# Kernel optimization log

Measured on AMD Instinct MI355X. Metric: run time of the kernel, lower is better.

Reference implementation:

```python
import jax, jax.numpy as jnp
import numpy as np

N_NODES = 100000
N_EDGES = 1600000
IN_DIM = 128
HID = 64
CONV2_OUT = 8
GLOBAL_DIM = 24
OUT_DIM = 1
NUM_GRAPHS = 64
NEG_SLOPE = 0.01


def setup_inputs() -> dict:
    key = jax.random.key(0)
    ks = jax.random.split(key, 12)
    x = jax.random.normal(ks[0], (N_NODES, IN_DIM), dtype=jnp.float32)
    edge_index = jax.random.randint(ks[1], (2, N_EDGES), 0, N_NODES, dtype=jnp.int32)
    batch = jnp.sort(jax.random.randint(ks[2], (N_NODES,), 0, NUM_GRAPHS, dtype=jnp.int32))
    global_features = jax.random.normal(ks[3], (NUM_GRAPHS, GLOBAL_DIM), dtype=jnp.float32)
    # GCNConv weights (glorot-ish scale) and Linear weights
    W1 = jax.random.normal(ks[4], (IN_DIM, HID), dtype=jnp.float32) / np.sqrt(IN_DIM)
    b1 = jnp.zeros((HID,), dtype=jnp.float32)
    W2 = jax.random.normal(ks[5], (HID, CONV2_OUT), dtype=jnp.float32) / np.sqrt(HID)
    b2 = jnp.zeros((CONV2_OUT,), dtype=jnp.float32)
    fcW1 = jax.random.normal(ks[6], (GLOBAL_DIM + CONV2_OUT, 16), dtype=jnp.float32) / np.sqrt(GLOBAL_DIM + CONV2_OUT)
    fcb1 = jnp.zeros((16,), dtype=jnp.float32)
    fcW2 = jax.random.normal(ks[7], (16, OUT_DIM), dtype=jnp.float32) / np.sqrt(16)
    fcb2 = jnp.zeros((OUT_DIM,), dtype=jnp.float32)
    return {"x": x, "edge_index": edge_index, "batch": batch,
            "global_features": global_features,
            "W1": W1, "b1": b1, "W2": W2, "b2": b2,
            "fcW1": fcW1, "fcb1": fcb1, "fcW2": fcW2, "fcb2": fcb2}


def gcn_conv(x, src, dst, W, b):
    """PyG GCNConv: add self-loops, sym-normalize, aggregate x@W from src->dst."""
    n = x.shape[0]
    h = x @ W  # [N, F_out]
    loop = jnp.arange(n, dtype=src.dtype)
    src2 = jnp.concatenate([src, loop])
    dst2 = jnp.concatenate([dst, loop])
    deg = jax.ops.segment_sum(jnp.ones_like(dst2, dtype=h.dtype), dst2, num_segments=n)
    dinv = jnp.where(deg > 0, jax.lax.rsqrt(deg), 0.0)
    norm = dinv[src2] * dinv[dst2]  # [E+N]
    msg = h[src2] * norm[:, None]   # edge gather (dominant traffic)
    out = jax.ops.segment_sum(msg, dst2, num_segments=n)
    return out + b


def reference(x, edge_index, batch, global_features, W1, b1, W2, b2, fcW1, fcb1, fcW2, fcb2):
    src, dst = edge_index[0], edge_index[1]
    h = jax.nn.leaky_relu(gcn_conv(x, src, dst, W1, b1), NEG_SLOPE)
    h = jax.nn.leaky_relu(gcn_conv(h, src, dst, W2, b2), NEG_SLOPE)
    # global mean pool over graphs
    sums = jax.ops.segment_sum(h, batch, num_segments=NUM_GRAPHS)
    cnts = jax.ops.segment_sum(jnp.ones((h.shape[0],), h.dtype), batch, num_segments=NUM_GRAPHS)
    pool = sums / jnp.maximum(cnts, 1.0)[:, None]
    z = jnp.concatenate([pool, global_features], axis=1)
    z = jax.nn.leaky_relu(z @ fcW1 + fcb1, NEG_SLOPE)
    z = jax.nn.leaky_relu(z @ fcW2 + fcb2, NEG_SLOPE)
    return z
```

## Files before the change

kernel.cpp:

```cpp
#include <hip/hip_runtime.h>

constexpr int N_NODES = 100000;
constexpr int N_EDGES = 1600000;
constexpr int IN_DIM  = 128;
constexpr int HID     = 64;
constexpr int C2      = 8;
constexpr int GDIM    = 24;
constexpr int NG      = 64;
constexpr float SLOPE = 0.01f;
constexpr int NB_SCAN = (N_NODES + 255) / 256;

__device__ __forceinline__ float lrelu(float v) { return v > 0.f ? v : SLOPE * v; }

__device__ __forceinline__ float bflo(unsigned int u) { return __uint_as_float(u << 16); }
__device__ __forceinline__ float bfhi(unsigned int u) { return __uint_as_float(u & 0xffff0000u); }
__device__ __forceinline__ unsigned short f2bf(float f) {
    unsigned int i = __float_as_uint(f);
    unsigned int r = (i + 0x7fffu + ((i >> 16) & 1u)) >> 16;
    return (unsigned short)r;
}

__global__ void k_rank(const int* __restrict__ dst, int* __restrict__ deg,
                       int* __restrict__ rnk) {
    int t = blockIdx.x * 256 + threadIdx.x;
    if (t < N_EDGES / 4) {
        int4 d = ((const int4*)dst)[t];
        int4 r;
        r.x = atomicAdd(&deg[d.x], 1);
        r.y = atomicAdd(&deg[d.y], 1);
        r.z = atomicAdd(&deg[d.z], 1);
        r.w = atomicAdd(&deg[d.w], 1);
        ((int4*)rnk)[t] = r;
    }
}

__global__ void k_scan1(const int* __restrict__ deg, int* __restrict__ rowptr,
                        int* __restrict__ bsum, float* __restrict__ dinv) {
    __shared__ int s[256];
    int tid = threadIdx.x;
    int i = blockIdx.x * 256 + tid;
    int v = (i < N_NODES) ? deg[i] : 0;
    if (i < N_NODES) dinv[i] = rsqrtf((float)(v + 1));
    s[tid] = v;
    __syncthreads();
    for (int off = 1; off < 256; off <<= 1) {
        int t = (tid >= off) ? s[tid - off] : 0;
        __syncthreads();
        s[tid] += t;
        __syncthreads();
    }
    if (i < N_NODES) rowptr[i] = s[tid] - v;
    if (tid == 255) bsum[blockIdx.x] = s[255];
}

__global__ void k_scan2(const int* __restrict__ bsum, int* __restrict__ bsumx) {
    __shared__ int s[512];
    int tid = threadIdx.x;
    int v = (tid < NB_SCAN) ? bsum[tid] : 0;
    s[tid] = v;
    __syncthreads();
    for (int off = 1; off < 512; off <<= 1) {
        int t = (tid >= off) ? s[tid - off] : 0;
        __syncthreads();
        s[tid] += t;
        __syncthreads();
    }
    if (tid < NB_SCAN) bsumx[tid] = s[tid] - v;
}

__global__ void k_place(const int* __restrict__ src, const int* __restrict__ dst,
                        const int* __restrict__ rnk, const int* __restrict__ rowptr,
                        const int* __restrict__ bsumx, int* __restrict__ eidx) {
    int t = blockIdx.x * 256 + threadIdx.x;
    if (t < N_EDGES / 4) {
        int4 d = ((const int4*)dst)[t];
        int4 r = ((const int4*)rnk)[t];
        int4 s = ((const int4*)src)[t];
        int px = rowptr[d.x] + bsumx[d.x >> 8] + r.x;
        int py = rowptr[d.y] + bsumx[d.y >> 8] + r.y;
        int pz = rowptr[d.z] + bsumx[d.z >> 8] + r.z;
        int pw = rowptr[d.w] + bsumx[d.w >> 8] + r.w;
        eidx[px] = s.x; eidx[py] = s.y; eidx[pz] = s.z; eidx[pw] = s.w;
    }
}

__global__ __launch_bounds__(256) void k_gemm1(const float* __restrict__ x,
                                               const float* __restrict__ W1,
                                               const float* __restrict__ dinv,
                                               unsigned short* __restrict__ hs1) {
    __shared__ float sW[IN_DIM * HID];
    __shared__ float sX[32][IN_DIM];
    int node0 = blockIdx.x * 32;
    for (int t = threadIdx.x; t < IN_DIM * HID / 4; t += 256)
        ((float4*)sW)[t] = ((const float4*)W1)[t];
    for (int t = threadIdx.x; t < 32 * IN_DIM / 4; t += 256) {
        int r = t >> 5, c4 = t & 31;
        ((float4*)&sX[r][0])[c4] = ((const float4*)(x + (size_t)(node0 + r) * IN_DIM))[c4];
    }
    __syncthreads();
    int col = threadIdx.x & 63;
    int nb  = (threadIdx.x >> 6) * 8;
    float acc[8] = {0.f, 0.f, 0.f, 0.f, 0.f, 0.f, 0.f, 0.f};
    for (int k4 = 0; k4 < IN_DIM; k4 += 4) {
        float w0 = sW[(k4 + 0) * HID + col];
        float w1 = sW[(k4 + 1) * HID + col];
        float w2 = sW[(k4 + 2) * HID + col];
        float w3 = sW[(k4 + 3) * HID + col];
#pragma unroll
        for (int j = 0; j < 8; ++j) {
            float4 xv = *((const float4*)&sX[nb + j][k4]);
            acc[j] += xv.x * w0 + xv.y * w1 + xv.z * w2 + xv.w * w3;
        }
    }
#pragma unroll
    for (int j = 0; j < 8; ++j) {
        int n = node0 + nb + j;
        hs1[(size_t)n * HID + col] = f2bf(acc[j] * dinv[n]);
    }
}

__global__ __launch_bounds__(256) void k_agg1(const int* __restrict__ rowptr,
                                              const int* __restrict__ bsumx,
                                              const int* __restrict__ deg,
                                              const int* __restrict__ eidx,
                                              const unsigned short* __restrict__ hs1,
                                              const float* __restrict__ dinv,
                                              const float* __restrict__ b1,
                                              const float* __restrict__ W2,
                                              float* __restrict__ hs2) {
    int node = blockIdx.x * 4 + (threadIdx.x >> 6);
    int lane = threadIdx.x & 63;
    int q    = lane & 7;
    int slot = lane >> 3;
    float w2f[8];
#pragma unroll
    for (int i = 0; i < 8; ++i) w2f[i] = W2[(8 * q + i) * C2 + slot];
    int start = rowptr[node] + bsumx[node >> 8];
    int cnt   = deg[node];
    uint4 hv = ((const uint4*)(hs1 + (size_t)node * HID))[q];
    float acc[8] = {0.f, 0.f, 0.f, 0.f, 0.f, 0.f, 0.f, 0.f};
    for (int base = 0; base < cnt; base += 64) {
        int idx = (base + lane < cnt) ? eidx[start + base + lane] : 0;
        int lim = min(64, cnt - base);
        int trips = (lim + 15) >> 4;
        for (int t = 0; t < trips; ++t) {
            int k0 = slot + t * 16;
            int k1 = k0 + 8;
            int s0 = __shfl(idx, k0);
            int s1 = __shfl(idx, k1 & 63);
            uint4 v0 = ((const uint4*)(hs1 + (size_t)s0 * HID))[q];
            uint4 v1 = ((const uint4*)(hs1 + (size_t)s1 * HID))[q];
            if (k0 >= lim) { v0.x = 0; v0.y = 0; v0.z = 0; v0.w = 0; }
            if (k1 >= lim) { v1.x = 0; v1.y = 0; v1.z = 0; v1.w = 0; }
            acc[0] += bflo(v0.x); acc[1] += bfhi(v0.x);
            acc[2] += bflo(v0.y); acc[3] += bfhi(v0.y);
            acc[4] += bflo(v0.z); acc[5] += bfhi(v0.z);
            acc[6] += bflo(v0.w); acc[7] += bfhi(v0.w);
            acc[0] += bflo(v1.x); acc[1] += bfhi(v1.x);
            acc[2] += bflo(v1.y); acc[3] += bfhi(v1.y);
            acc[4] += bflo(v1.z); acc[5] += bfhi(v1.z);
            acc[6] += bflo(v1.w); acc[7] += bfhi(v1.w);
        }
    }
#pragma unroll
    for (int m = 8; m < 64; m <<= 1)
#pragma unroll
        for (int i = 0; i < 8; ++i) acc[i] += __shfl_xor(acc[i], m);
    float self[8] = {bflo(hv.x), bfhi(hv.x), bflo(hv.y), bfhi(hv.y),
                     bflo(hv.z), bfhi(hv.z), bflo(hv.w), bfhi(hv.w)};
    float di = dinv[node];
    float4 bb0 = ((const float4*)b1)[2 * q];
    float4 bb1 = ((const float4*)b1)[2 * q + 1];
    float bv[8] = {bb0.x, bb0.y, bb0.z, bb0.w, bb1.x, bb1.y, bb1.z, bb1.w};
    float p = 0.f;
#pragma unroll
    for (int i = 0; i < 8; ++i) {
        float y = lrelu(di * (acc[i] + self[i]) + bv[i]);
        p += y * w2f[i];
    }
#pragma unroll
    for (int m = 1; m < 8; m <<= 1) p += __shfl_xor(p, m);
    if (q == 0) hs2[(size_t)node * C2 + slot] = p * di;
}

__global__ __launch_bounds__(256) void k_agg2(const int* __restrict__ rowptr,
                                              const int* __restrict__ bsumx,
                                              const int* __restrict__ deg,
                                              const int* __restrict__ eidx,
                                              const float* __restrict__ hs2,
                                              const float* __restrict__ dinv,
                                              const float* __restrict__ b2,
                                              float* __restrict__ y2) {
    int node = blockIdx.x * 4 + (threadIdx.x >> 6);
    int lane = threadIdx.x & 63;
    int q    = lane & 1;
    int slot = lane >> 1;
    int start = rowptr[node] + bsumx[node >> 8];
    int cnt   = deg[node];
    float4 acc = make_float4(0.f, 0.f, 0.f, 0.f);
    for (int base = 0; base < cnt; base += 64) {
        int idx = (base + lane < cnt) ? eidx[start + base + lane] : 0;
        int lim = min(64, cnt - base);
        int s0 = __shfl(idx, slot);
        int s1 = __shfl(idx, slot + 32);
        float4 v0 = ((const float4*)(hs2 + (size_t)s0 * C2))[q];
        float4 v1 = ((const float4*)(hs2 + (size_t)s1 * C2))[q];
        if (slot >= lim)      { v0.x = 0.f; v0.y = 0.f; v0.z = 0.f; v0.w = 0.f; }
        if (slot + 32 >= lim) { v1.x = 0.f; v1.y = 0.f; v1.z = 0.f; v1.w = 0.f; }
        acc.x += v0.x + v1.x; acc.y += v0.y + v1.y;
        acc.z += v0.z + v1.z; acc.w += v0.w + v1.w;
    }
    for (int m = 2; m < 64; m <<= 1) {
        acc.x += __shfl_xor(acc.x, m); acc.y += __shfl_xor(acc.y, m);
        acc.z += __shfl_xor(acc.z, m); acc.w += __shfl_xor(acc.w, m);
    }
    if (slot == 0) {
        float4 h = ((const float4*)(hs2 + (size_t)node * C2))[q];
        float di = dinv[node];
        const float* bb = b2 + q * 4;
        float4 r;
        r.x = lrelu(di * (acc.x + h.x) + bb[0]);
        r.y = lrelu(di * (acc.y + h.y) + bb[1]);
        r.z = lrelu(di * (acc.z + h.z) + bb[2]);
        r.w = lrelu(di * (acc.w + h.w) + bb[3]);
        ((float4*)(y2 + (size_t)node * C2))[q] = r;
    }
}

__device__ __forceinline__ int lower_bound(const int* __restrict__ b, int n, int v) {
    int lo = 0, hi = n;
    while (lo < hi) {
        int m = (lo + hi) >> 1;
        if (b[m] < v) lo = m + 1; else hi = m;
    }
    return lo;
}

__global__ __launch_bounds__(256) void k_pool(const float* __restrict__ y2,
                                              const int* __restrict__ batch,
                                              const float* __restrict__ gfeat,
                                              const float* __restrict__ fcW1,
                                              const float* __restrict__ fcb1,
                                              const float* __restrict__ fcW2,
                                              const float* __restrict__ fcb2,
                                              float* __restrict__ out) {
    __shared__ float s[256];
    int g   = blockIdx.x;
    int tid = threadIdx.x;
    int start = lower_bound(batch, N_NODES, g);
    int end   = lower_bound(batch, N_NODES, g + 1);
    int col = tid & 7;
    float local = 0.f;
    for (int n = start + (tid >> 3); n < end; n += 32)
        local += y2[(size_t)n * C2 + col];
    s[tid] = local;
    __syncthreads();
    for (int off = 128; off >= 8; off >>= 1) {
        if (tid < off) s[tid] += s[tid + off];
        __syncthreads();
    }
    if (tid == 0) {
        float cnt = fmaxf((float)(end - start), 1.f);
        float z[C2 + GDIM];
        for (int c = 0; c < C2; ++c) z[c] = s[c] / cnt;
        for (int c = 0; c < GDIM; ++c) z[C2 + c] = gfeat[g * GDIM + c];
        float acc2 = fcb2[0];
        for (int j = 0; j < 16; ++j) {
            float acc = fcb1[j];
            for (int c = 0; c < C2 + GDIM; ++c) acc += z[c] * fcW1[c * 16 + j];
            acc2 += lrelu(acc) * fcW2[j];
        }
        out[g] = lrelu(acc2);
    }
}

extern "C" void kernel_launch(void* const* d_in, const int* in_sizes, int n_in,
                              void* d_out, int out_size, void* d_ws, size_t ws_size,
                              hipStream_t stream) {
    const float* x     = (const float*)d_in[0];
    const int*   ei    = (const int*)d_in[1];
    const int*   batch = (const int*)d_in[2];
    const float* gfeat = (const float*)d_in[3];
    const float* W1    = (const float*)d_in[4];
    const float* b1    = (const float*)d_in[5];
    const float* W2    = (const float*)d_in[6];
    const float* b2    = (const float*)d_in[7];
    const float* fcW1  = (const float*)d_in[8];
    const float* fcb1  = (const float*)d_in[9];
    const float* fcW2  = (const float*)d_in[10];
    const float* fcb2  = (const float*)d_in[11];
    const int* src = ei;
    const int* dst = ei + N_EDGES;

    char* ws = (char*)d_ws;
    size_t off = 0;
    auto alloc = [&](size_t bytes) -> void* {
        void* p = ws + off;
        off = (off + bytes + 255) & ~(size_t)255;
        return p;
    };
    int*   deg    = (int*)  alloc((size_t)N_NODES * 4);
    float* dinv   = (float*)alloc((size_t)N_NODES * 4);
    int*   rowptr = (int*)  alloc((size_t)N_NODES * 4);
    int*   bsum   = (int*)  alloc(512 * 4);
    int*   bsumx  = (int*)  alloc(512 * 4);
    int*   rnk    = (int*)  alloc((size_t)N_EDGES * 4);
    int*   eidx   = (int*)  alloc((size_t)N_EDGES * 4);
    unsigned short* hs1 = (unsigned short*)alloc((size_t)N_NODES * HID * 2);
    float* hs2    = (float*)alloc((size_t)N_NODES * C2 * 4);
    float* y2     = (float*)alloc((size_t)N_NODES * C2 * 4);

    hipMemsetAsync(deg, 0, (size_t)N_NODES * 4, stream);

    k_rank <<<(N_EDGES / 4 + 255) / 256, 256, 0, stream>>>(dst, deg, rnk);
    k_scan1<<<NB_SCAN, 256, 0, stream>>>(deg, rowptr, bsum, dinv);
    k_scan2<<<1, 512, 0, stream>>>(bsum, bsumx);
    k_place<<<(N_EDGES / 4 + 255) / 256, 256, 0, stream>>>(src, dst, rnk, rowptr, bsumx, eidx);

    k_gemm1<<<N_NODES / 32, 256, 0, stream>>>(x, W1, dinv, hs1);
    k_agg1 <<<N_NODES / 4, 256, 0, stream>>>(rowptr, bsumx, deg, eidx, hs1, dinv, b1, W2, hs2);
    k_agg2 <<<N_NODES / 4, 256, 0, stream>>>(rowptr, bsumx, deg, eidx, hs2, dinv, b2, y2);
    k_pool <<<NG, 256, 0, stream>>>(y2, batch, gfeat, fcW1, fcb1, fcW2, fcb2, (float*)d_out);
}
```

Measured before the change: 283.9 us.

## Merge degree ranking with GEMM1 and edge placement with bf16 scaling

The edge rank/degree atomics now share a launch with the X@W1 GEMM, which no longer depends on dinv and writes unscaled fp32 output to a scratch buffer. A second combined kernel performs CSR edge placement alongside a vectorized pass that scales rows by dinv and packs them to bf16. The aim is to overlap atomic-bound and compute-bound work and to cut the number of kernel launches. The cost is an extra fp32 round trip of N×64 floats (about 25.6 MB written and read again). The GEMM also stops staging X in shared memory, and hs2/y2 now alias the scratch buffer.

Result: slower. 338.4 us (+19.2%).

```diff
diff --git a/kernel.cpp b/kernel.cpp
--- a/kernel.cpp
+++ b/kernel.cpp
@@ -9,29 +9,62 @@
 constexpr int NG      = 64;
 constexpr float SLOPE = 0.01f;
 constexpr int NB_SCAN = (N_NODES + 255) / 256;
+constexpr int RANK_BLOCKS  = (N_EDGES / 4 + 255) / 256;
+constexpr int GEMM_BLOCKS  = N_NODES / 32;
+constexpr int PLACE_BLOCKS = RANK_BLOCKS;
+constexpr int SCALE_BLOCKS = N_NODES * HID / 8 / 256;
 
 __device__ __forceinline__ float lrelu(float v) { return v > 0.f ? v : SLOPE * v; }
 
 __device__ __forceinline__ float bflo(unsigned int u) { return __uint_as_float(u << 16); }
 __device__ __forceinline__ float bfhi(unsigned int u) { return __uint_as_float(u & 0xffff0000u); }
-__device__ __forceinline__ unsigned short f2bf(float f) {
+__device__ __forceinline__ unsigned int f2bf_u(float f) {
     unsigned int i = __float_as_uint(f);
-    unsigned int r = (i + 0x7fffu + ((i >> 16) & 1u)) >> 16;
-    return (unsigned short)r;
-}
-
-__global__ void k_rank(const int* __restrict__ dst, int* __restrict__ deg,
-                       int* __restrict__ rnk) {
-    int t = blockIdx.x * 256 + threadIdx.x;
-    if (t < N_EDGES / 4) {
-        int4 d = ((const int4*)dst)[t];
-        int4 r;
-        r.x = atomicAdd(&deg[d.x], 1);
-        r.y = atomicAdd(&deg[d.y], 1);
-        r.z = atomicAdd(&deg[d.z], 1);
-        r.w = atomicAdd(&deg[d.w], 1);
-        ((int4*)rnk)[t] = r;
-    }
+    return (i + 0x7fffu + ((i >> 16) & 1u)) >> 16;
+}
+
+__global__ __launch_bounds__(256) void k_front(const float* __restrict__ x,
+                                               const float* __restrict__ W1,
+                                               const int* __restrict__ dst,
+                                               int* __restrict__ deg,
+                                               int* __restrict__ rnk,
+                                               float* __restrict__ raw) {
+    __shared__ float sW[IN_DIM * HID];
+    if (blockIdx.x < RANK_BLOCKS) {
+        int t = blockIdx.x * 256 + threadIdx.x;
+        if (t < N_EDGES / 4) {
+            int4 d = ((const int4*)dst)[t];
+            int4 r;
+            r.x = atomicAdd(&deg[d.x], 1);
+            r.y = atomicAdd(&deg[d.y], 1);
+            r.z = atomicAdd(&deg[d.z], 1);
+            r.w = atomicAdd(&deg[d.w], 1);
+            ((int4*)rnk)[t] = r;
+        }
+        return;
+    }
+    int node0 = (blockIdx.x - RANK_BLOCKS) * 32;
+    for (int t = threadIdx.x; t < IN_DIM * HID / 4; t += 256)
+        ((float4*)sW)[t] = ((const float4*)W1)[t];
+    __syncthreads();
+    int col = threadIdx.x & 63;
+    int nb  = (threadIdx.x >> 6) * 8;
+    const float* xb = x + (size_t)(node0 + nb) * IN_DIM;
+    float acc[8] = {0.f, 0.f, 0.f, 0.f, 0.f, 0.f, 0.f, 0.f};
+    for (int k4 = 0; k4 < IN_DIM; k4 += 4) {
+        float w0 = sW[(k4 + 0) * HID + col];
+        float w1 = sW[(k4 + 1) * HID + col];
+        float w2 = sW[(k4 + 2) * HID + col];
+        float w3 = sW[(k4 + 3) * HID + col];
+#pragma unroll
+        for (int j = 0; j < 8; ++j) {
+            float4 xv = *((const float4*)(xb + (size_t)j * IN_DIM + k4));
+            acc[j] += xv.x * w0 + xv.y * w1 + xv.z * w2 + xv.w * w3;
+        }
+    }
+#pragma unroll
+    for (int j = 0; j < 8; ++j)
+        raw[(size_t)(node0 + nb + j) * HID + col] = acc[j];
 }
 
 __global__ void k_scan1(const int* __restrict__ deg, int* __restrict__ rowptr,
@@ -68,55 +101,40 @@
     if (tid < NB_SCAN) bsumx[tid] = s[tid] - v;
 }
 
-__global__ void k_place(const int* __restrict__ src, const int* __restrict__ dst,
-                        const int* __restrict__ rnk, const int* __restrict__ rowptr,
-                        const int* __restrict__ bsumx, int* __restrict__ eidx) {
-    int t = blockIdx.x * 256 + threadIdx.x;
-    if (t < N_EDGES / 4) {
-        int4 d = ((const int4*)dst)[t];
-        int4 r = ((const int4*)rnk)[t];
-        int4 s = ((const int4*)src)[t];
-        int px = rowptr[d.x] + bsumx[d.x >> 8] + r.x;
-        int py = rowptr[d.y] + bsumx[d.y >> 8] + r.y;
-        int pz = rowptr[d.z] + bsumx[d.z >> 8] + r.z;
-        int pw = rowptr[d.w] + bsumx[d.w >> 8] + r.w;
-        eidx[px] = s.x; eidx[py] = s.y; eidx[pz] = s.z; eidx[pw] = s.w;
-    }
-}
-
-__global__ __launch_bounds__(256) void k_gemm1(const float* __restrict__ x,
-                                               const float* __restrict__ W1,
-                                               const float* __restrict__ dinv,
-                                               unsigned short* __restrict__ hs1) {
-    __shared__ float sW[IN_DIM * HID];
-    __shared__ float sX[32][IN_DIM];
-    int node0 = blockIdx.x * 32;
-    for (int t = threadIdx.x; t < IN_DIM * HID / 4; t += 256)
-        ((float4*)sW)[t] = ((const float4*)W1)[t];
-    for (int t = threadIdx.x; t < 32 * IN_DIM / 4; t += 256) {
-        int r = t >> 5, c4 = t & 31;
-        ((float4*)&sX[r][0])[c4] = ((const float4*)(x + (size_t)(node0 + r) * IN_DIM))[c4];
-    }
-    __syncthreads();
-    int col = threadIdx.x & 63;
-    int nb  = (threadIdx.x >> 6) * 8;
-    float acc[8] = {0.f, 0.f, 0.f, 0.f, 0.f, 0.f, 0.f, 0.f};
-    for (int k4 = 0; k4 < IN_DIM; k4 += 4) {
-        float w0 = sW[(k4 + 0) * HID + col];
-        float w1 = sW[(k4 + 1) * HID + col];
-        float w2 = sW[(k4 + 2) * HID + col];
-        float w3 = sW[(k4 + 3) * HID + col];
-#pragma unroll
-        for (int j = 0; j < 8; ++j) {
-            float4 xv = *((const float4*)&sX[nb + j][k4]);
-            acc[j] += xv.x * w0 + xv.y * w1 + xv.z * w2 + xv.w * w3;
-        }
-    }
-#pragma unroll
-    for (int j = 0; j < 8; ++j) {
-        int n = node0 + nb + j;
-        hs1[(size_t)n * HID + col] = f2bf(acc[j] * dinv[n]);
-    }
+__global__ __launch_bounds__(256) void k_mid(const int* __restrict__ src,
+                                             const int* __restrict__ dst,
+                                             const int* __restrict__ rnk,
+                                             const int* __restrict__ rowptr,
+                                             const int* __restrict__ bsumx,
+                                             int* __restrict__ eidx,
+                                             const float* __restrict__ raw,
+                                             const float* __restrict__ dinv,
+                                             unsigned short* __restrict__ hs1) {
+    if (blockIdx.x < PLACE_BLOCKS) {
+        int t = blockIdx.x * 256 + threadIdx.x;
+        if (t < N_EDGES / 4) {
+            int4 d = ((const int4*)dst)[t];
+            int4 r = ((const int4*)rnk)[t];
+            int4 s = ((const int4*)src)[t];
+            int px = rowptr[d.x] + bsumx[d.x >> 8] + r.x;
+            int py = rowptr[d.y] + bsumx[d.y >> 8] + r.y;
+            int pz = rowptr[d.z] + bsumx[d.z >> 8] + r.z;
+            int pw = rowptr[d.w] + bsumx[d.w >> 8] + r.w;
+            eidx[px] = s.x; eidx[py] = s.y; eidx[pz] = s.z; eidx[pw] = s.w;
+        }
+        return;
+    }
+    int t = (blockIdx.x - PLACE_BLOCKS) * 256 + threadIdx.x;
+    int node = t >> 3;
+    float di = dinv[node];
+    float4 a = ((const float4*)raw)[2 * t];
+    float4 b = ((const float4*)raw)[2 * t + 1];
+    uint4 o;
+    o.x = f2bf_u(a.x * di) | (f2bf_u(a.y * di) << 16);
+    o.y = f2bf_u(a.z * di) | (f2bf_u(a.w * di) << 16);
+    o.z = f2bf_u(b.x * di) | (f2bf_u(b.y * di) << 16);
+    o.w = f2bf_u(b.z * di) | (f2bf_u(b.w * di) << 16);
+    ((uint4*)hs1)[t] = o;
 }
 
 __global__ __launch_bounds__(256) void k_agg1(const int* __restrict__ rowptr,
@@ -307,17 +325,17 @@
     int*   rnk    = (int*)  alloc((size_t)N_EDGES * 4);
     int*   eidx   = (int*)  alloc((size_t)N_EDGES * 4);
     unsigned short* hs1 = (unsigned short*)alloc((size_t)N_NODES * HID * 2);
-    float* hs2    = (float*)alloc((size_t)N_NODES * C2 * 4);
-    float* y2     = (float*)alloc((size_t)N_NODES * C2 * 4);
+    float* raw    = (float*)alloc((size_t)N_NODES * HID * 4);
+    float* hs2 = raw;
+    float* y2  = raw + (size_t)N_NODES * C2;
 
     hipMemsetAsync(deg, 0, (size_t)N_NODES * 4, stream);
 
-    k_rank <<<(N_EDGES / 4 + 255) / 256, 256, 0, stream>>>(dst, deg, rnk);
+    k_front<<<RANK_BLOCKS + GEMM_BLOCKS, 256, 0, stream>>>(x, W1, dst, deg, rnk, raw);
     k_scan1<<<NB_SCAN, 256, 0, stream>>>(deg, rowptr, bsum, dinv);
     k_scan2<<<1, 512, 0, stream>>>(bsum, bsumx);
-    k_place<<<(N_EDGES / 4 + 255) / 256, 256, 0, stream>>>(src, dst, rnk, rowptr, bsumx, eidx);
-
-    k_gemm1<<<N_NODES / 32, 256, 0, stream>>>(x, W1, dinv, hs1);
+    k_mid  <<<PLACE_BLOCKS + SCALE_BLOCKS, 256, 0, stream>>>(src, dst, rnk, rowptr, bsumx,
+                                                             eidx, raw, dinv, hs1);
     k_agg1 <<<N_NODES / 4, 256, 0, stream>>>(rowptr, bsumx, deg, eidx, hs1, dinv, b1, W2, hs2);
     k_agg2 <<<N_NODES / 4, 256, 0, stream>>>(rowptr, bsumx, deg, eidx, hs2, dinv, b2, y2);
     k_pool <<<NG, 256, 0, stream>>>(y2, batch, gfeat, fcW1, fcb1, fcW2, fcb2, (float*)d_out);
```

## Fuse CSR scan via atomic block offsets and process eight nodes per wavefront

Applied to the files above, without the earlier changes.

The two-pass prefix scan becomes a single pass. Each block claims its base offset with an atomicAdd on a global counter, so the second scan kernel and the per-block sum lookups in the place and aggregation kernels go away. Row segments are still disjoint but are no longer in node order, which can reduce locality of the edge index reads. Separately, each wavefront in both aggregation kernels now handles eight nodes in a loop rather than one, cutting the block count eightfold. That trades launch and scheduling overhead against less parallelism and more load imbalance per wavefront.

Result: faster. 262.9 us (-7.4%).

```diff
diff --git a/kernel.cpp b/kernel.cpp
--- a/kernel.cpp
+++ b/kernel.cpp
@@ -20,26 +20,27 @@
     return (unsigned short)r;
 }
 
-__global__ void k_rank(const int* __restrict__ dst, int* __restrict__ deg,
+__global__ void k_rank(const int* __restrict__ dst, int* __restrict__ cnt,
                        int* __restrict__ rnk) {
     int t = blockIdx.x * 256 + threadIdx.x;
     if (t < N_EDGES / 4) {
         int4 d = ((const int4*)dst)[t];
         int4 r;
-        r.x = atomicAdd(&deg[d.x], 1);
-        r.y = atomicAdd(&deg[d.y], 1);
-        r.z = atomicAdd(&deg[d.z], 1);
-        r.w = atomicAdd(&deg[d.w], 1);
+        r.x = atomicAdd(&cnt[d.x], 1);
+        r.y = atomicAdd(&cnt[d.y], 1);
+        r.z = atomicAdd(&cnt[d.z], 1);
+        r.w = atomicAdd(&cnt[d.w], 1);
         ((int4*)rnk)[t] = r;
     }
 }
 
-__global__ void k_scan1(const int* __restrict__ deg, int* __restrict__ rowptr,
-                        int* __restrict__ bsum, float* __restrict__ dinv) {
+__global__ void k_scan1(const int* __restrict__ cnt, int* __restrict__ rowptr,
+                        float* __restrict__ dinv, int* __restrict__ gbase) {
     __shared__ int s[256];
+    __shared__ int base;
     int tid = threadIdx.x;
     int i = blockIdx.x * 256 + tid;
-    int v = (i < N_NODES) ? deg[i] : 0;
+    int v = (i < N_NODES) ? cnt[i] : 0;
     if (i < N_NODES) dinv[i] = rsqrtf((float)(v + 1));
     s[tid] = v;
     __syncthreads();
@@ -49,38 +50,23 @@
         s[tid] += t;
         __syncthreads();
     }
-    if (i < N_NODES) rowptr[i] = s[tid] - v;
-    if (tid == 255) bsum[blockIdx.x] = s[255];
-}
-
-__global__ void k_scan2(const int* __restrict__ bsum, int* __restrict__ bsumx) {
-    __shared__ int s[512];
-    int tid = threadIdx.x;
-    int v = (tid < NB_SCAN) ? bsum[tid] : 0;
-    s[tid] = v;
+    if (tid == 255) base = atomicAdd(gbase, s[255]);
     __syncthreads();
-    for (int off = 1; off < 512; off <<= 1) {
-        int t = (tid >= off) ? s[tid - off] : 0;
-        __syncthreads();
-        s[tid] += t;
-        __syncthreads();
-    }
-    if (tid < NB_SCAN) bsumx[tid] = s[tid] - v;
+    if (i < N_NODES) rowptr[i] = base + s[tid] - v;
 }
 
 __global__ void k_place(const int* __restrict__ src, const int* __restrict__ dst,
                         const int* __restrict__ rnk, const int* __restrict__ rowptr,
-                        const int* __restrict__ bsumx, int* __restrict__ eidx) {
+                        int* __restrict__ eidx) {
     int t = blockIdx.x * 256 + threadIdx.x;
     if (t < N_EDGES / 4) {
         int4 d = ((const int4*)dst)[t];
         int4 r = ((const int4*)rnk)[t];
         int4 s = ((const int4*)src)[t];
-        int px = rowptr[d.x] + bsumx[d.x >> 8] + r.x;
-        int py = rowptr[d.y] + bsumx[d.y >> 8] + r.y;
-        int pz = rowptr[d.z] + bsumx[d.z >> 8] + r.z;
-        int pw = rowptr[d.w] + bsumx[d.w >> 8] + r.w;
-        eidx[px] = s.x; eidx[py] = s.y; eidx[pz] = s.z; eidx[pw] = s.w;
+        eidx[rowptr[d.x] + r.x] = s.x;
+        eidx[rowptr[d.y] + r.y] = s.y;
+        eidx[rowptr[d.z] + r.z] = s.z;
+        eidx[rowptr[d.w] + r.w] = s.w;
     }
 }
 
@@ -120,7 +106,6 @@
 }
 
 __global__ __launch_bounds__(256) void k_agg1(const int* __restrict__ rowptr,
-                                              const int* __restrict__ bsumx,
                                               const int* __restrict__ deg,
                                               const int* __restrict__ eidx,
                                               const unsigned short* __restrict__ hs1,
@@ -128,102 +113,109 @@
                                               const float* __restrict__ b1,
                                               const float* __restrict__ W2,
                                               float* __restrict__ hs2) {
-    int node = blockIdx.x * 4 + (threadIdx.x >> 6);
     int lane = threadIdx.x & 63;
     int q    = lane & 7;
     int slot = lane >> 3;
     float w2f[8];
 #pragma unroll
     for (int i = 0; i < 8; ++i) w2f[i] = W2[(8 * q + i) * C2 + slot];
-    int start = rowptr[node] + bsumx[node >> 8];
-    int cnt   = deg[node];
-    uint4 hv = ((const uint4*)(hs1 + (size_t)node * HID))[q];
-    float acc[8] = {0.f, 0.f, 0.f, 0.f, 0.f, 0.f, 0.f, 0.f};
-    for (int base = 0; base < cnt; base += 64) {
-        int idx = (base + lane < cnt) ? eidx[start + base + lane] : 0;
-        int lim = min(64, cnt - base);
-        int trips = (lim + 15) >> 4;
-        for (int t = 0; t < trips; ++t) {
-            int k0 = slot + t * 16;
-            int k1 = k0 + 8;
-            int s0 = __shfl(idx, k0);
-            int s1 = __shfl(idx, k1 & 63);
-            uint4 v0 = ((const uint4*)(hs1 + (size_t)s0 * HID))[q];
-            uint4 v1 = ((const uint4*)(hs1 + (size_t)s1 * HID))[q];
-            if (k0 >= lim) { v0.x = 0; v0.y = 0; v0.z = 0; v0.w = 0; }
-            if (k1 >= lim) { v1.x = 0; v1.y = 0; v1.z = 0; v1.w = 0; }
-            acc[0] += bflo(v0.x); acc[1] += bfhi(v0.x);
-            acc[2] += bflo(v0.y); acc[3] += bfhi(v0.y);
-            acc[4] += bflo(v0.z); acc[5] += bfhi(v0.z);
-            acc[6] += bflo(v0.w); acc[7] += bfhi(v0.w);
-            acc[0] += bflo(v1.x); acc[1] += bfhi(v1.x);
-            acc[2] += bflo(v1.y); acc[3] += bfhi(v1.y);
-            acc[4] += bflo(v1.z); acc[5] += bfhi(v1.z);
-            acc[6] += bflo(v1.w); acc[7] += bfhi(v1.w);
-        }
-    }
-#pragma unroll
-    for (int m = 8; m < 64; m <<= 1)
-#pragma unroll
-        for (int i = 0; i < 8; ++i) acc[i] += __shfl_xor(acc[i], m);
-    float self[8] = {bflo(hv.x), bfhi(hv.x), bflo(hv.y), bfhi(hv.y),
-                     bflo(hv.z), bfhi(hv.z), bflo(hv.w), bfhi(hv.w)};
-    float di = dinv[node];
     float4 bb0 = ((const float4*)b1)[2 * q];
     float4 bb1 = ((const float4*)b1)[2 * q + 1];
     float bv[8] = {bb0.x, bb0.y, bb0.z, bb0.w, bb1.x, bb1.y, bb1.z, bb1.w};
-    float p = 0.f;
-#pragma unroll
-    for (int i = 0; i < 8; ++i) {
-        float y = lrelu(di * (acc[i] + self[i]) + bv[i]);
-        p += y * w2f[i];
-    }
-#pragma unroll
-    for (int m = 1; m < 8; m <<= 1) p += __shfl_xor(p, m);
-    if (q == 0) hs2[(size_t)node * C2 + slot] = p * di;
+    int node_base = blockIdx.x * 32 + (threadIdx.x >> 6) * 8;
+
+    for (int nn = 0; nn < 8; ++nn) {
+        int node  = node_base + nn;
+        int start = rowptr[node];
+        int cnt   = deg[node];
+        uint4 hv = ((const uint4*)(hs1 + (size_t)node * HID))[q];
+        float acc[8] = {0.f, 0.f, 0.f, 0.f, 0.f, 0.f, 0.f, 0.f};
+        for (int base = 0; base < cnt; base += 64) {
+            int idx = (base + lane < cnt) ? eidx[start + base + lane] : 0;
+            int lim = min(64, cnt - base);
+            int trips = (lim + 15) >> 4;
+            for (int t = 0; t < trips; ++t) {
+                int k0 = slot + t * 16;
+                int k1 = k0 + 8;
+                int s0 = __shfl(idx, k0);
+                int s1 = __shfl(idx, k1 & 63);
+                uint4 v0 = ((const uint4*)(hs1 + (size_t)s0 * HID))[q];
+                uint4 v1 = ((const uint4*)(hs1 + (size_t)s1 * HID))[q];
+                if (k0 >= lim) { v0.x = 0; v0.y = 0; v0.z = 0; v0.w = 0; }
+                if (k1 >= lim) { v1.x = 0; v1.y = 0; v1.z = 0; v1.w = 0; }
+                acc[0] += bflo(v0.x); acc[1] += bfhi(v0.x);
+                acc[2] += bflo(v0.y); acc[3] += bfhi(v0.y);
+                acc[4] += bflo(v0.z); acc[5] += bfhi(v0.z);
+                acc[6] += bflo(v0.w); acc[7] += bfhi(v0.w);
+                acc[0] += bflo(v1.x); acc[1] += bfhi(v1.x);
+                acc[2] += bflo(v1.y); acc[3] += bfhi(v1.y);
+                acc[4] += bflo(v1.z); acc[5] += bfhi(v1.z);
+                acc[6] += bflo(v1.w); acc[7] += bfhi(v1.w);
+            }
+        }
+#pragma unroll
+        for (int m = 8; m < 64; m <<= 1)
+#pragma unroll
+            for (int i = 0; i < 8; ++i) acc[i] += __shfl_xor(acc[i], m);
+        float self[8] = {bflo(hv.x), bfhi(hv.x), bflo(hv.y), bfhi(hv.y),
+                         bflo(hv.z), bfhi(hv.z), bflo(hv.w), bfhi(hv.w)};
+        float di = dinv[node];
+        float p = 0.f;
+#pragma unroll
+        for (int i = 0; i < 8; ++i) {
+            float y = lrelu(di * (acc[i] + self[i]) + bv[i]);
+            p += y * w2f[i];
+        }
+#pragma unroll
+        for (int m = 1; m < 8; m <<= 1) p += __shfl_xor(p, m);
+        if (q == 0) hs2[(size_t)node * C2 + slot] = p * di;
+    }
 }
 
 __global__ __launch_bounds__(256) void k_agg2(const int* __restrict__ rowptr,
-                                              const int* __restrict__ bsumx,
                                               const int* __restrict__ deg,
                                               const int* __restrict__ eidx,
                                               const float* __restrict__ hs2,
                                               const float* __restrict__ dinv,
                                               const float* __restrict__ b2,
                                               float* __restrict__ y2) {
-    int node = blockIdx.x * 4 + (threadIdx.x >> 6);
     int lane = threadIdx.x & 63;
     int q    = lane & 1;
     int slot = lane >> 1;
-    int start = rowptr[node] + bsumx[node >> 8];
-    int cnt   = deg[node];
-    float4 acc = make_float4(0.f, 0.f, 0.f, 0.f);
-    for (int base = 0; base < cnt; base += 64) {
-        int idx = (base + lane < cnt) ? eidx[start + base + lane] : 0;
-        int lim = min(64, cnt - base);
-        int s0 = __shfl(idx, slot);
-        int s1 = __shfl(idx, slot + 32);
-        float4 v0 = ((const float4*)(hs2 + (size_t)s0 * C2))[q];
-        float4 v1 = ((const float4*)(hs2 + (size_t)s1 * C2))[q];
-        if (slot >= lim)      { v0.x = 0.f; v0.y = 0.f; v0.z = 0.f; v0.w = 0.f; }
-        if (slot + 32 >= lim) { v1.x = 0.f; v1.y = 0.f; v1.z = 0.f; v1.w = 0.f; }
-        acc.x += v0.x + v1.x; acc.y += v0.y + v1.y;
-        acc.z += v0.z + v1.z; acc.w += v0.w + v1.w;
-    }
-    for (int m = 2; m < 64; m <<= 1) {
-        acc.x += __shfl_xor(acc.x, m); acc.y += __shfl_xor(acc.y, m);
-        acc.z += __shfl_xor(acc.z, m); acc.w += __shfl_xor(acc.w, m);
-    }
-    if (slot == 0) {
-        float4 h = ((const float4*)(hs2 + (size_t)node * C2))[q];
-        float di = dinv[node];
-        const float* bb = b2 + q * 4;
-        float4 r;
-        r.x = lrelu(di * (acc.x + h.x) + bb[0]);
-        r.y = lrelu(di * (acc.y + h.y) + bb[1]);
-        r.z = lrelu(di * (acc.z + h.z) + bb[2]);
-        r.w = lrelu(di * (acc.w + h.w) + bb[3]);
-        ((float4*)(y2 + (size_t)node * C2))[q] = r;
+    int node_base = blockIdx.x * 32 + (threadIdx.x >> 6) * 8;
+
+    for (int nn = 0; nn < 8; ++nn) {
+        int node  = node_base + nn;
+        int start = rowptr[node];
+        int cnt   = deg[node];
+        float4 acc = make_float4(0.f, 0.f, 0.f, 0.f);
+        for (int base = 0; base < cnt; base += 64) {
+            int idx = (base + lane < cnt) ? eidx[start + base + lane] : 0;
+            int lim = min(64, cnt - base);
+            int s0 = __shfl(idx, slot);
+            int s1 = __shfl(idx, slot + 32);
+            float4 v0 = ((const float4*)(hs2 + (size_t)s0 * C2))[q];
+            float4 v1 = ((const float4*)(hs2 + (size_t)s1 * C2))[q];
+            if (slot >= lim)      { v0.x = 0.f; v0.y = 0.f; v0.z = 0.f; v0.w = 0.f; }
+            if (slot + 32 >= lim) { v1.x = 0.f; v1.y = 0.f; v1.z = 0.f; v1.w = 0.f; }
+            acc.x += v0.x + v1.x; acc.y += v0.y + v1.y;
+            acc.z += v0.z + v1.z; acc.w += v0.w + v1.w;
+        }
+        for (int m = 2; m < 64; m <<= 1) {
+            acc.x += __shfl_xor(acc.x, m); acc.y += __shfl_xor(acc.y, m);
+            acc.z += __shfl_xor(acc.z, m); acc.w += __shfl_xor(acc.w, m);
+        }
+        if (slot == 0) {
+            float4 h = ((const float4*)(hs2 + (size_t)node * C2))[q];
+            float di = dinv[node];
+            const float* bb = b2 + q * 4;
+            float4 r;
+            r.x = lrelu(di * (acc.x + h.x) + bb[0]);
+            r.y = lrelu(di * (acc.y + h.y) + bb[1]);
+            r.z = lrelu(di * (acc.z + h.z) + bb[2]);
+            r.w = lrelu(di * (acc.w + h.w) + bb[3]);
+            ((float4*)(y2 + (size_t)node * C2))[q] = r;
+        }
     }
 }
 
@@ -299,26 +291,24 @@
         off = (off + bytes + 255) & ~(size_t)255;
         return p;
     };
-    int*   deg    = (int*)  alloc((size_t)N_NODES * 4);
+    int*   cnt    = (int*)  alloc((size_t)N_NODES * 4 + 256);
+    int*   gbase  = cnt + N_NODES;
     float* dinv   = (float*)alloc((size_t)N_NODES * 4);
     int*   rowptr = (int*)  alloc((size_t)N_NODES * 4);
-    int*   bsum   = (int*)  alloc(512 * 4);
-    int*   bsumx  = (int*)  alloc(512 * 4);
     int*   rnk    = (int*)  alloc((size_t)N_EDGES * 4);
     int*   eidx   = (int*)  alloc((size_t)N_EDGES * 4);
     unsigned short* hs1 = (unsigned short*)alloc((size_t)N_NODES * HID * 2);
     float* hs2    = (float*)alloc((size_t)N_NODES * C2 * 4);
     float* y2     = (float*)alloc((size_t)N_NODES * C2 * 4);
 
-    hipMemsetAsync(deg, 0, (size_t)N_NODES * 4, stream);
-
-    k_rank <<<(N_EDGES / 4 + 255) / 256, 256, 0, stream>>>(dst, deg, rnk);
-    k_scan1<<<NB_SCAN, 256, 0, stream>>>(deg, rowptr, bsum, dinv);
-    k_scan2<<<1, 512, 0, stream>>>(bsum, bsumx);
-    k_place<<<(N_EDGES / 4 + 255) / 256, 256, 0, stream>>>(src, dst, rnk, rowptr, bsumx, eidx);
+    hipMemsetAsync(cnt, 0, (size_t)N_NODES * 4 + 256, stream);
+
+    k_rank <<<(N_EDGES / 4 + 255) / 256, 256, 0, stream>>>(dst, cnt, rnk);
+    k_scan1<<<NB_SCAN, 256, 0, stream>>>(cnt, rowptr, dinv, gbase);
+    k_place<<<(N_EDGES / 4 + 255) / 256, 256, 0, stream>>>(src, dst, rnk, rowptr, eidx);
 
     k_gemm1<<<N_NODES / 32, 256, 0, stream>>>(x, W1, dinv, hs1);
-    k_agg1 <<<N_NODES / 4, 256, 0, stream>>>(rowptr, bsumx, deg, eidx, hs1, dinv, b1, W2, hs2);
-    k_agg2 <<<N_NODES / 4, 256, 0, stream>>>(rowptr, bsumx, deg, eidx, hs2, dinv, b2, y2);
+    k_agg1 <<<N_NODES / 32, 256, 0, stream>>>(rowptr, cnt, eidx, hs1, dinv, b1, W2, hs2);
+    k_agg2 <<<N_NODES / 32, 256, 0, stream>>>(rowptr, cnt, eidx, hs2, dinv, b2, y2);
     k_pool <<<NG, 256, 0, stream>>>(y2, batch, gfeat, fcW1, fcb1, fcW2, fcb2, (float*)d_out);
 }
```
